# Kernel optimization log

Hardware: AMD Instinct MI355X
Metric: run time of the kernel (lower is better)

## Reference

```python
import jax, jax.numpy as jnp
import numpy as np
from jax import lax

N, D = 8, 32            # batch, map_depth
S = 2                   # belief_downsample_factor
HS, WS = 512, 512       # semantic map resolution
H, W = HS // S, WS // S # belief resolution (256, 256)
K = 7                   # motion_kernel_size
KK = K * K
HID = 64                # motion_hidden_size
A = 256                 # action_embedding_size


def _conv(x, w, b, pad, dil=1):
    # x: NCHW, w: OIHW
    y = lax.conv_general_dilated(
        x, w, window_strides=(1, 1), padding=[(pad, pad), (pad, pad)],
        rhs_dilation=(dil, dil), dimension_numbers=('NCHW', 'OIHW', 'NCHW'))
    return y + b[None, :, None, None]


def _unfold_index():
    # Reproduces nn.Unfold([K,K]) applied to ConstantPad2d(K//2, -1)(arange image).
    # Result flattened in (ki*K+kj, i, j) order, matching col2im flatten order.
    pad = K // 2
    img = np.arange(H * W, dtype=np.int64).reshape(H, W)
    imgp = np.pad(img, ((pad, pad), (pad, pad)), constant_values=-1)
    idx = np.empty((K, K, H, W), dtype=np.int64)
    for ki in range(K):
        for kj in range(K):
            idx[ki, kj] = imgp[ki:ki + H, kj:kj + W]
    return idx.reshape(-1)  # (K*K*H*W,)

_IDX = _unfold_index()
_VALID = _IDX >= 0
_IDX_SAFE = np.where(_VALID, _IDX, 0)


def _scatter_logsumexp(src, idx, num_segments):
    # src: (B, M) with -inf marking invalid entries; idx: (M,) shared across B.
    def one(s):
        mx = jax.ops.segment_max(s, idx, num_segments=num_segments)          # (P,)
        g = mx[idx]                                                          # (M,)
        contrib = jnp.where(jnp.isneginf(s), 0.0,
                            jnp.exp(s - jnp.where(jnp.isfinite(g), g, 0.0)))
        sm = jax.ops.segment_sum(contrib, idx, num_segments=num_segments)    # (P,)
        return mx + jnp.log(jnp.where(jnp.isfinite(mx), sm, 1.0))
    return jax.vmap(one)(src)


def setup_inputs() -> dict:
    key = jax.random.key(0)
    ks = jax.random.split(key, 20)
    f32 = jnp.float32
    return {
        'log_belief': jax.random.normal(ks[0], (N, 1, H, W), f32),
        'semantic_map': jax.random.normal(ks[1], (N, D, HS, WS), f32),
        'action': jax.random.normal(ks[2], (N, A), f32),
        # Bottleneck(map_depth -> hidden -> map_depth, dilations [3,1])
        'w_in': jax.random.normal(ks[3], (HID, D, 1, 1), f32) * 0.1,
        'b_in': jnp.zeros((HID,), f32),
        'w_d3': jax.random.normal(ks[4], (HID, HID, 3, 3), f32) * 0.05,
        'b_d3': jnp.zeros((HID,), f32),
        'w_d1': jax.random.normal(ks[5], (HID, HID, 3, 3), f32) * 0.05,
        'b_d1': jnp.zeros((HID,), f32),
        'w_out': jax.random.normal(ks[6], (D, HID, 1, 1), f32) * 0.1,
        'b_out': jnp.zeros((D,), f32),
        # conv1x1: map_depth -> K*K
        'w_k': jax.random.normal(ks[7], (KK, D, 1, 1), f32) * 0.1,
        'b_k': jnp.zeros((KK,), f32),
        # DenseMlpBlock2: A -> hidden -> K*K
        'w_a1': jax.random.normal(ks[8], (A, HID), f32) * 0.05,
        'b_a1': jnp.zeros((HID,), f32),
        'w_a2': jax.random.normal(ks[9], (HID, KK), f32) * 0.05,
        'b_a2': jnp.zeros((KK,), f32),
    }


def reference(log_belief, semantic_map, action,
              w_in, b_in, w_d3, b_d3, w_d1, b_d1, w_out, b_out,
              w_k, b_k, w_a1, b_a1, w_a2, b_a2):
    # Dropout in eval mode -> identity. MaxPool2d(S, stride=S):
    x = lax.reduce_window(semantic_map, -jnp.inf, lax.max,
                          (1, 1, S, S), (1, 1, S, S), 'VALID')  # (N,D,H,W)
    # Bottleneck (conv1x1 -> dilated 3x3 convs -> conv1x1, residual)
    h = jax.nn.relu(_conv(x, w_in, b_in, 0))
    h = jax.nn.relu(_conv(h, w_d3, b_d3, 3, 3))
    h = jax.nn.relu(_conv(h, w_d1, b_d1, 1, 1))
    x2 = x + _conv(h, w_out, b_out, 0)
    # motion kernel logits over K*K taps per pixel
    motion = jax.nn.log_softmax(_conv(x2, w_k, b_k, 0), axis=1)   # (N,KK,H,W)
    lang = jax.nn.log_softmax(
        jax.nn.relu(action @ w_a1 + b_a1) @ w_a2 + b_a2, axis=1)  # (N,KK)
    log_kernel = jax.nn.log_softmax(motion + lang[:, :, None, None], axis=1)
    # propagate_belief: col2im + scatter_logsumexp (C=1, Cin=Cout=1)
    src = (log_belief + log_kernel).reshape(N, -1)                # (N, KK*H*W)
    idx = jnp.asarray(_IDX_SAFE)
    src = jnp.where(jnp.asarray(_VALID)[None, :], src, -jnp.inf)
    new_belief = _scatter_logsumexp(src, idx, H * W)              # (N, H*W)
    return new_belief.reshape(N, 1, H, W)
```

## Files before the change

kernel.cpp:

```cpp
#include <hip/hip_runtime.h>
#include <hip/hip_bf16.h>

typedef __hip_bfloat16 bf16;
typedef _Float16 fp16;
typedef __attribute__((ext_vector_type(8)))  short  short8;
typedef __attribute__((ext_vector_type(16))) float  floatx16;

#define HW 65536

__device__ __forceinline__ bf16  f2b(float v){ return __float2bfloat16(v); }
__device__ __forceinline__ unsigned short f2bu(float v){
  union { bf16 h; unsigned short u; } cv; cv.h = __float2bfloat16(v); return cv.u;
}
__device__ __forceinline__ float bu2f(unsigned short u){
  union { unsigned u; float f; } cv; cv.u = ((unsigned)u) << 16; return cv.f;
}
__device__ __forceinline__ unsigned short f2hu(float v){
  union { fp16 h; unsigned short u; } cv; cv.h = (fp16)v; return cv.u;
}
__device__ __forceinline__ float hu2f(unsigned short u){
  union { fp16 h; unsigned short u; } cv; cv.u = u; return (float)cv.h;
}

__global__ __launch_bounds__(256) void setup_pool_kernel(
    const float* __restrict__ sm, const float* __restrict__ w_in,
    const float* __restrict__ b_in, fp16* __restrict__ x, bf16* __restrict__ h1,
    const float* __restrict__ w_d3, const float* __restrict__ w_d1,
    bf16* __restrict__ wb3, bf16* __restrict__ wb1,
    const float* __restrict__ action,
    const float* __restrict__ w_a1, const float* __restrict__ b_a1,
    const float* __restrict__ w_a2, const float* __restrict__ b_a2,
    float* __restrict__ lang){
  int blk = blockIdx.x;
  if (blk < 2048){
    int p = blk*256 + threadIdx.x;
    int n = p >> 16; int ij = p & 65535; int i = ij >> 8; int j = ij & 255;
    const float* smn = sm + ((long)n << 23);
    float xv[32];
    #pragma unroll
    for (int d = 0; d < 32; d++){
      long base = ((long)(d*512 + 2*i) << 9) + 2*j;
      float2 p0 = *reinterpret_cast<const float2*>(smn + base);
      float2 p1 = *reinterpret_cast<const float2*>(smn + base + 512);
      xv[d] = fmaxf(fmaxf(p0.x, p0.y), fmaxf(p1.x, p1.y));
    }
    unsigned xw[16];
    #pragma unroll
    for (int q = 0; q < 16; q++)
      xw[q] = ((unsigned)f2hu(xv[2*q+1]) << 16) | f2hu(xv[2*q]);
    uint4* xo = reinterpret_cast<uint4*>((char*)x + ((long)p << 6));
    #pragma unroll
    for (int q = 0; q < 4; q++)
      xo[q] = make_uint4(xw[4*q], xw[4*q+1], xw[4*q+2], xw[4*q+3]);
    unsigned ow[32];
    #pragma unroll 4
    for (int c = 0; c < 64; c += 2){
      float a0 = b_in[c], a1 = b_in[c+1];
      #pragma unroll
      for (int d = 0; d < 32; d++){
        a0 += xv[d]*w_in[c*32+d];
        a1 += xv[d]*w_in[(c+1)*32+d];
      }
      ow[c>>1] = ((unsigned)f2bu(fmaxf(a1,0.f)) << 16) | f2bu(fmaxf(a0,0.f));
    }
    uint4* ho = reinterpret_cast<uint4*>((char*)h1 + ((long)p << 7));
    #pragma unroll
    for (int q = 0; q < 8; q++)
      ho[q] = make_uint4(ow[4*q], ow[4*q+1], ow[4*q+2], ow[4*q+3]);
  } else {
    int b = blk - 2048;
    if (b < 288){
      const float* w = (b < 144) ? w_d3 : w_d1;
      bf16* wb = (b < 144) ? wb3 : wb1;
      int i = (b < 144 ? b : b - 144)*256 + threadIdx.x;
      if (i >= 36864) return;
      int j    = i & 7;
      int gran = i >> 3;
      int col  = gran & 63;
      int oc   = ((col & 31) << 1) | (col >> 5);
      int rest = gran >> 6;
      int half = rest & 1;
      int ks   = (rest >> 1) & 3;
      int t    = rest >> 3;
      int e  = ks*16 + half*8 + j;
      int ki = t / 3, kj = t - ki*3;
      wb[i] = f2b(w[(oc*64 + e)*9 + ki*3 + kj]);
    } else {
      int n = b - 288;
      int t = threadIdx.x;
      __shared__ float part[256];
      __shared__ float hid[64];
      int d = t & 63, q = t >> 6;
      const float* ar = action + n*256;
      float a = 0.f;
      #pragma unroll 8
      for (int i = q*64; i < q*64 + 64; i++) a += ar[i]*w_a1[i*64 + d];
      part[t] = a;
      __syncthreads();
      if (t < 64)
        hid[t] = fmaxf(b_a1[t] + part[t] + part[64+t] + part[128+t] + part[192+t], 0.f);
      __syncthreads();
      if (t < 49){
        float l = b_a2[t];
        #pragma unroll 8
        for (int j2 = 0; j2 < 64; j2++) l += hid[j2]*w_a2[j2*49 + t];
        lang[n*49 + t] = l;
      }
    }
  }
}

template<int DIL>
__global__ __launch_bounds__(256) void conv3x3_mfma(
    const bf16* __restrict__ hin, const bf16* __restrict__ wb,
    const float* __restrict__ bias, bf16* __restrict__ hout){
  constexpr int R = 16 + 2*DIL, C = 16 + 2*DIL, NPIX = R*C;
  __shared__ __align__(16) char tile[NPIX*128];
  int b = blockIdx.x;
  int n = b & 7; int tb = b >> 3;
  int i0 = (tb >> 4) << 4, j0 = (tb & 15) << 4;
  int tid = threadIdx.x;
  const bf16* hn = hin + ((long)n << 22);
  for (int s = tid; s < NPIX*8; s += 256){
    int pix = s >> 3, g = s & 7;
    int r = pix / C, c = pix - r*C;
    int gi = i0 - DIL + r, gj = j0 - DIL + c;
    uint4 v = make_uint4(0u,0u,0u,0u);
    if (gi >= 0 && gi < 256 && gj >= 0 && gj < 256)
      v = *reinterpret_cast<const uint4*>(hn + (((long)((gi<<8) + gj)) << 6) + (g<<3));
    *reinterpret_cast<uint4*>(tile + pix*128 + ((g ^ (pix & 7)) << 4)) = v;
  }
  __syncthreads();
  int lane = tid & 63, wv = tid >> 6;
  int l31 = lane & 31, half = lane >> 5;
  floatx16 acc[2][2];
  #pragma unroll
  for (int m2 = 0; m2 < 2; m2++){
    acc[m2][0] = (floatx16)(0.0f);
    acc[m2][1] = (floatx16)(0.0f);
  }
  int prr[2], pcc[2];
  #pragma unroll
  for (int m2 = 0; m2 < 2; m2++){
    int pidx = (wv*2 + m2)*32 + l31;
    prr[m2] = pidx >> 4; pcc[m2] = pidx & 15;
  }
  const char* wbc = reinterpret_cast<const char*>(wb);
  for (int t = 0; t < 9; t++){
    int ki = t / 3, kj = t - ki*3;
    int pp[2];
    #pragma unroll
    for (int m2 = 0; m2 < 2; m2++)
      pp[m2] = (prr[m2] + ki*DIL)*C + (pcc[m2] + kj*DIL);
    short8 bfr[4][2];
    #pragma unroll
    for (int ks = 0; ks < 4; ks++){
      #pragma unroll
      for (int nt = 0; nt < 2; nt++)
        bfr[ks][nt] = *reinterpret_cast<const short8*>(
            wbc + ((((t*4 + ks)*2 + half)*64 + nt*32 + l31) << 4));
    }
    #pragma unroll
    for (int ks = 0; ks < 4; ks++){
      #pragma unroll
      for (int m2 = 0; m2 < 2; m2++){
        short8 afrag = *reinterpret_cast<const short8*>(
            tile + pp[m2]*128 + (((ks*2 + half) ^ (pp[m2] & 7)) << 4));
        acc[m2][0] = __builtin_amdgcn_mfma_f32_32x32x16_bf16(afrag, bfr[ks][0], acc[m2][0], 0, 0, 0);
        acc[m2][1] = __builtin_amdgcn_mfma_f32_32x32x16_bf16(afrag, bfr[ks][1], acc[m2][1], 0, 0, 0);
      }
    }
  }
  float bv0 = bias[2*l31], bv1 = bias[2*l31+1];
  bf16* ho = hout + ((long)n << 22);
  #pragma unroll
  for (int m2 = 0; m2 < 2; m2++){
    #pragma unroll
    for (int reg = 0; reg < 16; reg++){
      int row = (reg & 3) + 8*(reg >> 2) + 4*half;
      int pidx = (wv*2 + m2)*32 + row;
      int pr = pidx >> 4, pc = pidx & 15;
      int off = ((i0+pr)<<8) + (j0+pc);
      unsigned pk = ((unsigned)f2bu(fmaxf(acc[m2][1][reg] + bv1, 0.f)) << 16)
                  |  f2bu(fmaxf(acc[m2][0][reg] + bv0, 0.f));
      *reinterpret_cast<unsigned*>((char*)ho + (((long)off) << 7) + (l31 << 2)) = pk;
    }
  }
}

__global__ __launch_bounds__(256) void out_motion_kernel(
    const bf16* __restrict__ h3, const fp16* __restrict__ x,
    const float* __restrict__ w_out, const float* __restrict__ b_out,
    const float* __restrict__ w_k, const float* __restrict__ b_k,
    const float* __restrict__ lang, fp16* __restrict__ lk){
  int p = blockIdx.x*256 + threadIdx.x;
  int n = p >> 16; int ij = p & 65535;
  float hv[64];
  const uint4* hp = reinterpret_cast<const uint4*>((const char*)h3 + ((long)p << 7));
  #pragma unroll
  for (int q = 0; q < 8; q++){
    uint4 u = hp[q];
    unsigned uu[4] = {u.x, u.y, u.z, u.w};
    #pragma unroll
    for (int k = 0; k < 4; k++){
      hv[q*8 + 2*k]   = bu2f((unsigned short)(uu[k] & 0xffffu));
      hv[q*8 + 2*k+1] = bu2f((unsigned short)(uu[k] >> 16));
    }
  }
  float o[32];
  const uint4* xp = reinterpret_cast<const uint4*>((const char*)x + ((long)p << 6));
  #pragma unroll
  for (int q = 0; q < 4; q++){
    uint4 u = xp[q];
    unsigned uu[4] = {u.x, u.y, u.z, u.w};
    #pragma unroll
    for (int k = 0; k < 4; k++){
      o[q*8 + 2*k]   = hu2f((unsigned short)(uu[k] & 0xffffu));
      o[q*8 + 2*k+1] = hu2f((unsigned short)(uu[k] >> 16));
    }
  }
  #pragma unroll 4
  for (int d = 0; d < 32; d++){
    float acc = b_out[d];
    #pragma unroll
    for (int e = 0; e < 64; e++) acc += hv[e]*w_out[d*64+e];
    o[d] += acc;
  }
  float lg[49]; float m = -1e30f;
  #pragma unroll 7
  for (int k = 0; k < 49; k++){
    float acc = b_k[k] + lang[n*49+k];
    #pragma unroll
    for (int d = 0; d < 32; d++) acc += o[d]*w_k[k*32+d];
    lg[k] = acc; m = fmaxf(m, acc);
  }
  float s = 0.f;
  #pragma unroll
  for (int k = 0; k < 49; k++) s += __expf(lg[k]-m);
  float lse = m + __logf(s);
  #pragma unroll
  for (int k = 0; k < 49; k++)
    lk[(long)n*49*HW + (long)k*HW + ij] = (fp16)(lg[k] - lse);
}

__global__ __launch_bounds__(256) void gather_lse_kernel(
    const float* __restrict__ lb, const fp16* __restrict__ lk, float* __restrict__ out){
  int b = blockIdx.x;
  int n = b & 7;
  int ij = ((b >> 3) << 8) | threadIdx.x;
  int i = ij >> 8; int j = ij & 255;
  const fp16* lkn = lk + (long)n*49*HW;
  float v[49]; float m = -1e30f;
  #pragma unroll
  for (int ki = 0; ki < 7; ki++){
    int h = i + 3 - ki;
    bool hok = (h >= 0 && h < 256);
    #pragma unroll
    for (int kj = 0; kj < 7; kj++){
      int w = j + 3 - kj;
      float val = -1e30f;
      if (hok && w >= 0 && w < 256){
        int q = h*256 + w;
        val = lb[n*HW + q] + (float)lkn[(ki*7+kj)*HW + q];
      }
      v[ki*7+kj] = val; m = fmaxf(m, val);
    }
  }
  float s = 0.f;
  #pragma unroll
  for (int t = 0; t < 49; t++) s += __expf(v[t]-m);
  out[n*HW + ij] = m + __logf(s);
}

extern "C" void kernel_launch(void* const* d_in, const int* in_sizes, int n_in,
                              void* d_out, int out_size, void* d_ws, size_t ws_size,
                              hipStream_t stream) {
  (void)in_sizes; (void)n_in; (void)out_size; (void)ws_size;
  const float* lb    = (const float*)d_in[0];
  const float* sm    = (const float*)d_in[1];
  const float* act   = (const float*)d_in[2];
  const float* w_in  = (const float*)d_in[3];
  const float* b_in  = (const float*)d_in[4];
  const float* w_d3  = (const float*)d_in[5];
  const float* b_d3  = (const float*)d_in[6];
  const float* w_d1  = (const float*)d_in[7];
  const float* b_d1  = (const float*)d_in[8];
  const float* w_out = (const float*)d_in[9];
  const float* b_out = (const float*)d_in[10];
  const float* w_k   = (const float*)d_in[11];
  const float* b_k   = (const float*)d_in[12];
  const float* w_a1  = (const float*)d_in[13];
  const float* b_a1  = (const float*)d_in[14];
  const float* w_a2  = (const float*)d_in[15];
  const float* b_a2  = (const float*)d_in[16];
  float* out = (float*)d_out;

  char* ws = (char*)d_ws;
  fp16*  x    = (fp16*) (ws + 0);
  bf16*  h1   = (bf16*) (ws + 67108864);
  bf16*  h2   = (bf16*) (ws + 134217728);
  fp16*  lk   = (fp16*) (ws + 134217728);
  float* lang = (float*)(ws + 236978176);
  bf16*  wb3  = (bf16*) (ws + 236979968);
  bf16*  wb1  = (bf16*) (ws + 237053696);

  setup_pool_kernel<<<2344, 256, 0, stream>>>(sm, w_in, b_in, x, h1,
                                              w_d3, w_d1, wb3, wb1,
                                              act, w_a1, b_a1, w_a2, b_a2, lang);
  conv3x3_mfma<3><<<2048, 256, 0, stream>>>(h1, wb3, b_d3, h2);
  conv3x3_mfma<1><<<2048, 256, 0, stream>>>(h2, wb1, b_d1, h1);
  out_motion_kernel<<<2048, 256, 0, stream>>>(h1, x, w_out, b_out,
                                              w_k, b_k, lang, lk);
  gather_lse_kernel<<<2048, 256, 0, stream>>>(lb, lk, out);
}
```

Baseline: 662.0 us.

## Split conv3x3 MFMA work across 8 waves with one M-tile per wave

The dilated 3x3 conv kernels now launch 512 threads per block instead of 256, and each wave computes one 32-pixel M tile instead of two. This halves the accumulator registers per wave and adds waves for latency hiding, and the halo tile load is spread over more threads. In exchange, each B-fragment weight load is reused by only one MFMA pair rather than two, which raises weight-load traffic per FLOP.

```diff
diff --git a/kernel.cpp b/kernel.cpp
--- a/kernel.cpp
+++ b/kernel.cpp
@@ -111,7 +111,7 @@
 }
 
 template<int DIL>
-__global__ __launch_bounds__(256) void conv3x3_mfma(
+__global__ __launch_bounds__(512, 4) void conv3x3_mfma(
     const bf16* __restrict__ hin, const bf16* __restrict__ wb,
     const float* __restrict__ bias, bf16* __restrict__ hout){
   constexpr int R = 16 + 2*DIL, C = 16 + 2*DIL, NPIX = R*C;
@@ -121,7 +121,7 @@
   int i0 = (tb >> 4) << 4, j0 = (tb & 15) << 4;
   int tid = threadIdx.x;
   const bf16* hn = hin + ((long)n << 22);
-  for (int s = tid; s < NPIX*8; s += 256){
+  for (int s = tid; s < NPIX*8; s += 512){
     int pix = s >> 3, g = s & 7;
     int r = pix / C, c = pix - r*C;
     int gi = i0 - DIL + r, gj = j0 - DIL + c;
@@ -133,25 +133,14 @@
   __syncthreads();
   int lane = tid & 63, wv = tid >> 6;
   int l31 = lane & 31, half = lane >> 5;
-  floatx16 acc[2][2];
-  #pragma unroll
-  for (int m2 = 0; m2 < 2; m2++){
-    acc[m2][0] = (floatx16)(0.0f);
-    acc[m2][1] = (floatx16)(0.0f);
-  }
-  int prr[2], pcc[2];
-  #pragma unroll
-  for (int m2 = 0; m2 < 2; m2++){
-    int pidx = (wv*2 + m2)*32 + l31;
-    prr[m2] = pidx >> 4; pcc[m2] = pidx & 15;
-  }
+  floatx16 acc0 = (floatx16)(0.0f);
+  floatx16 acc1 = (floatx16)(0.0f);
+  int pidx = wv*32 + l31;
+  int prr = pidx >> 4, pcc = pidx & 15;
   const char* wbc = reinterpret_cast<const char*>(wb);
   for (int t = 0; t < 9; t++){
     int ki = t / 3, kj = t - ki*3;
-    int pp[2];
-    #pragma unroll
-    for (int m2 = 0; m2 < 2; m2++)
-      pp[m2] = (prr[m2] + ki*DIL)*C + (pcc[m2] + kj*DIL);
+    int pp = (prr + ki*DIL)*C + (pcc + kj*DIL);
     short8 bfr[4][2];
     #pragma unroll
     for (int ks = 0; ks < 4; ks++){
@@ -162,29 +151,23 @@
     }
     #pragma unroll
     for (int ks = 0; ks < 4; ks++){
-      #pragma unroll
-      for (int m2 = 0; m2 < 2; m2++){
-        short8 afrag = *reinterpret_cast<const short8*>(
-            tile + pp[m2]*128 + (((ks*2 + half) ^ (pp[m2] & 7)) << 4));
-        acc[m2][0] = __builtin_amdgcn_mfma_f32_32x32x16_bf16(afrag, bfr[ks][0], acc[m2][0], 0, 0, 0);
-        acc[m2][1] = __builtin_amdgcn_mfma_f32_32x32x16_bf16(afrag, bfr[ks][1], acc[m2][1], 0, 0, 0);
-      }
+      short8 afrag = *reinterpret_cast<const short8*>(
+          tile + pp*128 + (((ks*2 + half) ^ (pp & 7)) << 4));
+      acc0 = __builtin_amdgcn_mfma_f32_32x32x16_bf16(afrag, bfr[ks][0], acc0, 0, 0, 0);
+      acc1 = __builtin_amdgcn_mfma_f32_32x32x16_bf16(afrag, bfr[ks][1], acc1, 0, 0, 0);
     }
   }
   float bv0 = bias[2*l31], bv1 = bias[2*l31+1];
   bf16* ho = hout + ((long)n << 22);
   #pragma unroll
-  for (int m2 = 0; m2 < 2; m2++){
-    #pragma unroll
-    for (int reg = 0; reg < 16; reg++){
-      int row = (reg & 3) + 8*(reg >> 2) + 4*half;
-      int pidx = (wv*2 + m2)*32 + row;
-      int pr = pidx >> 4, pc = pidx & 15;
-      int off = ((i0+pr)<<8) + (j0+pc);
-      unsigned pk = ((unsigned)f2bu(fmaxf(acc[m2][1][reg] + bv1, 0.f)) << 16)
-                  |  f2bu(fmaxf(acc[m2][0][reg] + bv0, 0.f));
-      *reinterpret_cast<unsigned*>((char*)ho + (((long)off) << 7) + (l31 << 2)) = pk;
-    }
+  for (int reg = 0; reg < 16; reg++){
+    int row = (reg & 3) + 8*(reg >> 2) + 4*half;
+    int po = wv*32 + row;
+    int pr = po >> 4, pc = po & 15;
+    int off = ((i0+pr)<<8) + (j0+pc);
+    unsigned pk = ((unsigned)f2bu(fmaxf(acc1[reg] + bv1, 0.f)) << 16)
+                |  f2bu(fmaxf(acc0[reg] + bv0, 0.f));
+    *reinterpret_cast<unsigned*>((char*)ho + (((long)off) << 7) + (l31 << 2)) = pk;
   }
 }
 
@@ -307,8 +290,8 @@
   setup_pool_kernel<<<2344, 256, 0, stream>>>(sm, w_in, b_in, x, h1,
                                               w_d3, w_d1, wb3, wb1,
                                               act, w_a1, b_a1, w_a2, b_a2, lang);
-  conv3x3_mfma<3><<<2048, 256, 0, stream>>>(h1, wb3, b_d3, h2);
-  conv3x3_mfma<1><<<2048, 256, 0, stream>>>(h2, wb1, b_d1, h1);
+  conv3x3_mfma<3><<<2048, 512, 0, stream>>>(h1, wb3, b_d3, h2);
+  conv3x3_mfma<1><<<2048, 512, 0, stream>>>(h2, wb1, b_d1, h1);
   out_motion_kernel<<<2048, 256, 0, stream>>>(h1, x, w_out, b_out,
                                               w_k, b_k, lang, lk);
   gather_lse_kernel<<<2048, 256, 0, stream>>>(lb, lk, out);
```

After: 652.5 us. Within noise of the previous version (-1.4%).
